# Kernel tuning notes

Hardware: AMD Instinct MI355X
Metric: run time of the kernel (lower is better)

## Reference

```python
import jax, jax.numpy as jnp
import numpy as np

H, DH = 8, 64          # heads, dim_head
SCALE = DH ** -0.5

def _ln(x, g, b, eps=1e-5):
    m = jnp.mean(x, axis=-1, keepdims=True)
    v = jnp.var(x, axis=-1, keepdims=True)
    return (x - m) / jnp.sqrt(v + eps) * g + b

def setup_inputs() -> dict:
    key = jax.random.key(0)
    ks = jax.random.split(key, 16)
    b, n, din, dim, depth, mlp, nc = 4, 2048, 768, 512, 2, 512, 2
    s = 0.02
    x = jax.random.normal(ks[0], (b, n, din), jnp.float32)
    lens = jax.random.randint(ks[1], (b,), n // 2, n + 1)
    lens = lens.at[0].set(n)  # ensure amax(lens) == n so torch's truncation is a no-op
    return {
        "x": x,
        "lens": lens,
        "cls_token": jax.random.normal(ks[2], (1, 1, dim), jnp.float32),
        "fc_w": jax.random.normal(ks[3], (din, dim), jnp.float32) * s,
        "fc_b": jnp.zeros((dim,), jnp.float32),
        "ln1_g": jnp.ones((depth, dim), jnp.float32),
        "ln1_b": jnp.zeros((depth, dim), jnp.float32),
        "qkv_w": jax.random.normal(ks[4], (depth, dim, 3 * H * DH), jnp.float32) * s,
        "out_w": jax.random.normal(ks[5], (depth, H * DH, dim), jnp.float32) * s,
        "out_b": jnp.zeros((depth, dim), jnp.float32),
        "ln2_g": jnp.ones((depth, dim), jnp.float32),
        "ln2_b": jnp.zeros((depth, dim), jnp.float32),
        "ff1_w": jax.random.normal(ks[6], (depth, dim, mlp), jnp.float32) * s,
        "ff1_b": jnp.zeros((depth, mlp), jnp.float32),
        "ff2_w": jax.random.normal(ks[7], (depth, mlp, dim), jnp.float32) * s,
        "ff2_b": jnp.zeros((depth, dim), jnp.float32),
        "lnf_g": jnp.ones((dim,), jnp.float32),
        "lnf_b": jnp.zeros((dim,), jnp.float32),
        "head_w": jax.random.normal(ks[8], (dim, nc), jnp.float32) * s,
        "head_b": jnp.zeros((nc,), jnp.float32),
    }

def reference(x, lens, cls_token, fc_w, fc_b, ln1_g, ln1_b, qkv_w, out_w, out_b,
              ln2_g, ln2_b, ff1_w, ff1_b, ff2_w, ff2_b, lnf_g, lnf_b, head_w, head_b):
    b, n, _ = x.shape
    # fc + GELU (exact erf gelu, matching torch nn.GELU default)
    x = jax.nn.gelu(x @ fc_w + fc_b, approximate=False)
    x = jnp.concatenate([jnp.broadcast_to(cls_token, (b, 1, x.shape[-1])), x], axis=1)
    n1 = n + 1
    lens1 = lens + 1
    # faithful mask: mask @ mask.mT -> True only where BOTH query and key are padding
    pad = jnp.arange(n1)[None, :] >= lens1[:, None]           # [b, n1]
    mask2 = pad[:, :, None] & pad[:, None, :]                  # [b, n1, n1]
    neg = -jnp.finfo(x.dtype).max
    depth = qkv_w.shape[0]
    for l in range(depth):
        xn = _ln(x, ln1_g[l], ln1_b[l])
        qkv = xn @ qkv_w[l]                                    # [b, n1, 3*H*DH]
        q, k, v = jnp.split(qkv, 3, axis=-1)
        q = q.reshape(b, n1, H, DH).transpose(0, 2, 1, 3)      # [b, h, n1, dh]
        k = k.reshape(b, n1, H, DH).transpose(0, 2, 1, 3)
        v = v.reshape(b, n1, H, DH).transpose(0, 2, 1, 3)
        dots = jnp.einsum('bhid,bhjd->bhij', q, k) * SCALE
        dots = jnp.where(mask2[:, None], neg, dots)
        dots = dots - jnp.max(dots, axis=-1, keepdims=True)
        attn = jax.nn.softmax(dots, axis=-1)
        o = jnp.einsum('bhij,bhjd->bhid', attn, v)
        o = o.transpose(0, 2, 1, 3).reshape(b, n1, H * DH)
        x = o @ out_w[l] + out_b[l] + x
        h = jax.nn.gelu(_ln(x, ln2_g[l], ln2_b[l]) @ ff1_w[l] + ff1_b[l], approximate=False)
        x = h @ ff2_w[l] + ff2_b[l] + x
    x = _ln(x, lnf_g, lnf_b)
    return x[:, 0] @ head_w + head_b   # pool='cls'
```

## Files before the change

kernel.cpp:

```cpp
#include <hip/hip_runtime.h>
#include <hip/hip_bf16.h>
#include <math.h>
#include <float.h>

typedef __hip_bfloat16 bf16;
using bf16x8 = __attribute__((ext_vector_type(8))) __bf16;
using f32x4  = __attribute__((ext_vector_type(4))) float;

constexpr int BATCH = 4;
constexpr int SEQ   = 2048;
constexpr int SEQ1  = 2049;
constexpr int DIN   = 768;
constexpr int DIMC  = 512;
constexpr int DEPTH = 2;
constexpr int NHEAD = 8;
constexpr int DHEAD = 64;
constexpr int ROWS  = BATCH * SEQ1;
constexpr int VKP   = 2112;
constexpr float ATT_SCALE = 0.125f;
constexpr float NEGBIG = -1e30f;

__device__ __forceinline__ bf16x8 ld_frag(const bf16* p) { return *(const bf16x8*)p; }

__device__ __forceinline__ void g2lds16(const bf16* g, bf16* l) {
    __builtin_amdgcn_global_load_lds(
        (const __attribute__((address_space(1))) void*)g,
        (__attribute__((address_space(3))) void*)l, 16, 0, 0);
}

__global__ __launch_bounds__(256) void cast_kernel(const float* __restrict__ src,
                                                   bf16* __restrict__ dst, int n4) {
    int i = blockIdx.x * 256 + threadIdx.x;
    if (i < n4) {
        float4 v = ((const float4*)src)[i];
        dst[i * 4 + 0] = __float2bfloat16(v.x);
        dst[i * 4 + 1] = __float2bfloat16(v.y);
        dst[i * 4 + 2] = __float2bfloat16(v.z);
        dst[i * 4 + 3] = __float2bfloat16(v.w);
    }
}

__global__ __launch_bounds__(256) void wt_transpose_kernel(
    const float* __restrict__ src, bf16* __restrict__ dst,
    int R, int C, long zstride) {
    __shared__ bf16 tile[32][33];
    int z = blockIdx.z;
    const float* s = src + (size_t)z * zstride;
    bf16* d = dst + (size_t)z * zstride;
    int tx = threadIdx.x, ty = threadIdx.y;
    int c0 = blockIdx.x * 32, r0 = blockIdx.y * 32;
    int c = c0 + tx;
#pragma unroll
    for (int rr = ty; rr < 32; rr += 8) {
        int r = r0 + rr;
        tile[rr][tx] = (r < R && c < C) ? __float2bfloat16(s[(size_t)r * C + c])
                                        : __float2bfloat16(0.f);
    }
    __syncthreads();
    int rc = r0 + tx;
#pragma unroll
    for (int cc = ty; cc < 32; cc += 8) {
        int oc = c0 + cc;
        if (rc < R && oc < C) d[(size_t)oc * R + rc] = tile[tx][cc];
    }
}

__global__ __launch_bounds__(256) void vt_transpose_kernel(
    const bf16* __restrict__ QKV, bf16* __restrict__ VT) {
    __shared__ bf16 tile[32][33];
    int z = blockIdx.z;
    int bb = z >> 3, hh = z & 7;
    const bf16* s = QKV + (size_t)bb * SEQ1 * 1536 + 1024 + hh * 64;
    bf16* d = VT + (size_t)z * 64 * VKP;
    int tx = threadIdx.x, ty = threadIdx.y;
    int c0 = blockIdx.x * 32, r0 = blockIdx.y * 32;
    int c = c0 + tx;
#pragma unroll
    for (int rr = ty; rr < 32; rr += 8) {
        int r = r0 + rr;
        tile[rr][tx] = (r < SEQ1) ? s[(size_t)r * 1536 + c] : __float2bfloat16(0.f);
    }
    __syncthreads();
    int rc = r0 + tx;
#pragma unroll
    for (int cc = ty; cc < 32; cc += 8) {
        int oc = c0 + cc;
        if (rc < VKP) d[(size_t)oc * VKP + rc] = tile[tx][cc];
    }
}

__global__ void cls_fill_kernel(const float* __restrict__ cls, float* __restrict__ X) {
    int b = blockIdx.x;
    for (int d = threadIdx.x; d < DIMC; d += blockDim.x)
        X[(size_t)b * SEQ1 * DIMC + d] = cls[d];
}

template<int BM, bool GELU_, bool RESID, bool REMAP, bool OBF>
__global__ __launch_bounds__(256) void gemm_bt(
    const bf16* __restrict__ A, const bf16* __restrict__ Bt,
    const float* __restrict__ bias, const float* __restrict__ resid,
    float* __restrict__ Cf, bf16* __restrict__ Ch, int M, int N, int K) {
    constexpr int MI = BM / 32;
    __shared__ __align__(16) bf16 As[BM * 32];
    __shared__ __align__(16) bf16 Bs[4096];
    int tid = threadIdx.x;
    int ln = tid & 63, wv = tid >> 6;
    int wr = wv >> 1, wc = wv & 1;
    int l15 = ln & 15, l4 = ln >> 4;
    int m0 = blockIdx.y * BM, n0 = blockIdx.x * 128;

    f32x4 acc[MI][4];
#pragma unroll
    for (int i = 0; i < MI; ++i)
#pragma unroll
        for (int j = 0; j < 4; ++j) acc[i][j] = {0.f, 0.f, 0.f, 0.f};

    int aslot[MI], bslot[4];
#pragma unroll
    for (int i = 0; i < MI; ++i) {
        int m = wr * (BM / 2) + i * 16 + l15;
        aslot[i] = m * 4 + (l4 ^ ((m >> 1) & 3));
    }
#pragma unroll
    for (int j = 0; j < 4; ++j) {
        int n = wc * 64 + j * 16 + l15;
        bslot[j] = n * 4 + (l4 ^ ((n >> 1) & 3));
    }

    for (int k0 = 0; k0 < K; k0 += 32) {
#pragma unroll
        for (int r = 0; r < BM / 64; ++r) {
            int s = r * 256 + tid;
            int m = s >> 2, c = s & 3;
            int kb = c ^ ((m >> 1) & 3);
            int gm = m0 + m; if (gm > M - 1) gm = M - 1;
            g2lds16(A + (size_t)gm * K + k0 + kb * 8, &As[s * 8]);
        }
#pragma unroll
        for (int r = 0; r < 2; ++r) {
            int s = r * 256 + tid;
            int n = s >> 2, c = s & 3;
            int kb = c ^ ((n >> 1) & 3);
            g2lds16(Bt + (size_t)(n0 + n) * K + k0 + kb * 8, &Bs[s * 8]);
        }
        __syncthreads();
        bf16x8 af[MI], bfr[4];
#pragma unroll
        for (int i = 0; i < MI; ++i) af[i] = ld_frag(&As[aslot[i] * 8]);
#pragma unroll
        for (int j = 0; j < 4; ++j) bfr[j] = ld_frag(&Bs[bslot[j] * 8]);
#pragma unroll
        for (int i = 0; i < MI; ++i)
#pragma unroll
            for (int j = 0; j < 4; ++j)
                acc[i][j] = __builtin_amdgcn_mfma_f32_16x16x32_bf16(af[i], bfr[j], acc[i][j], 0, 0, 0);
        __syncthreads();
    }

#pragma unroll
    for (int i = 0; i < MI; ++i) {
#pragma unroll
        for (int j = 0; j < 4; ++j) {
            int gn = n0 + wc * 64 + j * 16 + l15;
            float bb = bias ? bias[gn] : 0.f;
#pragma unroll
            for (int r = 0; r < 4; ++r) {
                int gm = m0 + wr * (BM / 2) + i * 16 + l4 * 4 + r;
                if (gm >= M) continue;
                float v = acc[i][j][r] + bb;
                if (GELU_) v = 0.5f * v * (1.f + erff(v * 0.70710678118654752f));
                size_t orow = gm;
                if (REMAP) { int b_ = gm >> 11; orow = (size_t)b_ * SEQ1 + (gm & 2047) + 1; }
                size_t oi = orow * (size_t)N + gn;
                if (RESID) v += resid[oi];
                if (OBF) Ch[oi] = __float2bfloat16(v); else Cf[oi] = v;
            }
        }
    }
}

__global__ __launch_bounds__(256) void ln_kernel(const float* __restrict__ Xin, bf16* __restrict__ Xout,
                          const float* __restrict__ g, const float* __restrict__ bb) {
    int wv = threadIdx.x >> 6, ln = threadIdx.x & 63;
    int row = blockIdx.x * 4 + wv;
    if (row >= ROWS) return;
    const float* xr = Xin + (size_t)row * DIMC + ln * 8;
    float4 a = *(const float4*)xr;
    float4 c = *(const float4*)(xr + 4);
    float s = a.x + a.y + a.z + a.w + c.x + c.y + c.z + c.w;
#pragma unroll
    for (int off = 1; off < 64; off <<= 1) s += __shfl_xor(s, off, 64);
    float mean = s * (1.f / 512.f);
    float d[8] = {a.x - mean, a.y - mean, a.z - mean, a.w - mean,
                  c.x - mean, c.y - mean, c.z - mean, c.w - mean};
    float var = 0.f;
#pragma unroll
    for (int e = 0; e < 8; ++e) var += d[e] * d[e];
#pragma unroll
    for (int off = 1; off < 64; off <<= 1) var += __shfl_xor(var, off, 64);
    float rinv = rsqrtf(var * (1.f / 512.f) + 1e-5f);
    const float* gp = g + ln * 8;
    const float* bp = bb + ln * 8;
    float4 g0 = *(const float4*)gp, g1 = *(const float4*)(gp + 4);
    float4 b0 = *(const float4*)bp, b1 = *(const float4*)(bp + 4);
    float gg[8] = {g0.x, g0.y, g0.z, g0.w, g1.x, g1.y, g1.z, g1.w};
    float bbv[8] = {b0.x, b0.y, b0.z, b0.w, b1.x, b1.y, b1.z, b1.w};
    union { unsigned short u[8]; uint4 v; } ou;
#pragma unroll
    for (int e = 0; e < 8; ++e)
        ou.u[e] = __builtin_bit_cast(unsigned short, __float2bfloat16(d[e] * rinv * gg[e] + bbv[e]));
    *(uint4*)(Xout + (size_t)row * DIMC + ln * 8) = ou.v;
}

__global__ __launch_bounds__(256, 5) void attn_kernel(
    const bf16* __restrict__ QKV, const bf16* __restrict__ VT,
    const int* __restrict__ lens, bf16* __restrict__ O) {
    __shared__ __align__(16) bf16 Ks[2][4096];
    __shared__ __align__(16) bf16 Vs[2][4096];
    int tid = threadIdx.x, ln = tid & 63, wv = tid >> 6;
    int l15 = ln & 15, l4 = ln >> 4;
    int q0 = blockIdx.x * 64, h = blockIdx.y, b = blockIdx.z;
    int len1 = lens[b] + 1;
    const bf16* qkv_b = QKV + (size_t)b * SEQ1 * 1536;
    const bf16* vt_b  = VT + (size_t)(b * 8 + h) * 64 * VKP;

    uint4 z4 = make_uint4(0u, 0u, 0u, 0u);
    uint4 q0v = z4, q1v = z4;
    int qrow = q0 + wv * 16 + l15;
    if (qrow < SEQ1) {
        const bf16* qp = qkv_b + (size_t)qrow * 1536 + h * 64 + l4 * 8;
        q0v = *(const uint4*)qp;
        q1v = *(const uint4*)(qp + 32);
    }
    bf16x8 bq0 = __builtin_bit_cast(bf16x8, q0v);
    bf16x8 bq1 = __builtin_bit_cast(bf16x8, q1v);
    bool qpad = (qrow >= len1);

    float mrun = NEGBIG, lrun = 0.f;
    f32x4 oaccT[4];
#pragma unroll
    for (int t = 0; t < 4; ++t) oaccT[t] = {0.f, 0.f, 0.f, 0.f};

    uint4 kr[2], vr[2];
    int srow[2], sseg[2];
    int kslot[2], vslot[2];
#pragma unroll
    for (int rr = 0; rr < 2; ++rr) {
        int idx = rr * 256 + tid;
        int row = idx >> 3, seg = idx & 7;
        srow[rr] = row; sseg[rr] = seg;
        int pb = row >> 5, w = row & 31;
        int krow = pb * 32 + ((w >> 2) & 1) * 16 + (w >> 3) * 4 + (w & 3);
        kslot[rr] = krow * 8 + (seg ^ (krow & 7));
        vslot[rr] = row * 8 + (seg ^ (row & 7));
    }

#pragma unroll
    for (int rr = 0; rr < 2; ++rr) {
        kr[rr] = (srow[rr] < SEQ1)
            ? *(const uint4*)(qkv_b + (size_t)srow[rr] * 1536 + 512 + h * 64 + sseg[rr] * 8) : z4;
        vr[rr] = *(const uint4*)(vt_b + (size_t)srow[rr] * VKP + sseg[rr] * 8);
    }
#pragma unroll
    for (int rr = 0; rr < 2; ++rr) {
        *(uint4*)&Ks[0][kslot[rr] * 8] = kr[rr];
        *(uint4*)&Vs[0][vslot[rr] * 8] = vr[rr];
    }
    __syncthreads();

    for (int kt = 0; kt < 33; ++kt) {
        int k0 = kt * 64;
        int buf = kt & 1;
        if (kt < 32) {
            int kn = k0 + 64;
#pragma unroll
            for (int rr = 0; rr < 2; ++rr) {
                kr[rr] = (kn + srow[rr] < SEQ1)
                    ? *(const uint4*)(qkv_b + (size_t)(kn + srow[rr]) * 1536 + 512 + h * 64 + sseg[rr] * 8) : z4;
                vr[rr] = *(const uint4*)(vt_b + (size_t)srow[rr] * VKP + kn + sseg[rr] * 8);
            }
        }

        f32x4 sacc[2][2];
#pragma unroll
        for (int pb = 0; pb < 2; ++pb)
#pragma unroll
            for (int s = 0; s < 2; ++s) {
                int R = pb * 32 + s * 16 + l15;
                f32x4 a = {0.f, 0.f, 0.f, 0.f};
                bf16x8 kf0 = ld_frag(&Ks[buf][(R * 8 + (l4 ^ (R & 7))) * 8]);
                bf16x8 kf1 = ld_frag(&Ks[buf][(R * 8 + ((l4 + 4) ^ (R & 7))) * 8]);
                a = __builtin_amdgcn_mfma_f32_16x16x32_bf16(kf0, bq0, a, 0, 0, 0);
                a = __builtin_amdgcn_mfma_f32_16x16x32_bf16(kf1, bq1, a, 0, 0, 0);
                sacc[pb][s] = a;
            }

        bool needmask = (k0 + 64 > len1) || (kt == 32);
        float sv[2][2][4];
        float mx = NEGBIG;
#pragma unroll
        for (int pb = 0; pb < 2; ++pb)
#pragma unroll
            for (int s = 0; s < 2; ++s)
#pragma unroll
                for (int r = 0; r < 4; ++r) {
                    float v = sacc[pb][s][r] * ATT_SCALE;
                    if (needmask) {
                        int j = k0 + pb * 32 + l4 * 8 + s * 4 + r;
                        if (j >= SEQ1 || (qpad && j >= len1)) v = NEGBIG;
                    }
                    sv[pb][s][r] = v;
                    mx = fmaxf(mx, v);
                }
        mx = fmaxf(mx, __shfl_xor(mx, 16, 64));
        mx = fmaxf(mx, __shfl_xor(mx, 32, 64));
        float mnew = fmaxf(mrun, mx);
        float alpha = __expf(mrun - mnew);
        float rs = 0.f;
        unsigned short pk[2][8];
#pragma unroll
        for (int pb = 0; pb < 2; ++pb)
#pragma unroll
            for (int s = 0; s < 2; ++s)
#pragma unroll
                for (int r = 0; r < 4; ++r) {
                    float ex = sv[pb][s][r] - mnew;
                    float p = (ex < -80.f) ? 0.f : __expf(ex);
                    rs += p;
                    pk[pb][s * 4 + r] = __builtin_bit_cast(unsigned short, __float2bfloat16(p));
                }
        rs += __shfl_xor(rs, 16, 64);
        rs += __shfl_xor(rs, 32, 64);
        lrun = lrun * alpha + rs;
        mrun = mnew;
#pragma unroll
        for (int t = 0; t < 4; ++t) {
            oaccT[t][0] *= alpha; oaccT[t][1] *= alpha;
            oaccT[t][2] *= alpha; oaccT[t][3] *= alpha;
        }

#pragma unroll
        for (int pb = 0; pb < 2; ++pb) {
            union { unsigned short u[8]; bf16x8 v; } pu;
#pragma unroll
            for (int e = 0; e < 8; ++e) pu.u[e] = pk[pb][e];
            bf16x8 pf = pu.v;
#pragma unroll
            for (int t = 0; t < 4; ++t) {
                int VR = t * 16 + l15;
                bf16x8 vf = ld_frag(&Vs[buf][(VR * 8 + ((pb * 4 + l4) ^ (VR & 7))) * 8]);
                oaccT[t] = __builtin_amdgcn_mfma_f32_16x16x32_bf16(vf, pf, oaccT[t], 0, 0, 0);
            }
        }

        if (kt < 32) {
            int ob = buf ^ 1;
#pragma unroll
            for (int rr = 0; rr < 2; ++rr) {
                *(uint4*)&Ks[ob][kslot[rr] * 8] = kr[rr];
                *(uint4*)&Vs[ob][vslot[rr] * 8] = vr[rr];
            }
        }
        __syncthreads();
    }

    if (qrow < SEQ1) {
        float rl = (lrun > 0.f) ? 1.f / lrun : 0.f;
        bf16* orow = O + ((size_t)b * SEQ1 + qrow) * DIMC + h * 64;
#pragma unroll
        for (int t = 0; t < 4; ++t) {
            union { unsigned short u[4]; uint2 v; } ou;
#pragma unroll
            for (int r = 0; r < 4; ++r)
                ou.u[r] = __builtin_bit_cast(unsigned short, __float2bfloat16(oaccT[t][r] * rl));
            *(uint2*)&orow[t * 16 + l4 * 4] = ou.v;
        }
    }
}

__global__ __launch_bounds__(256) void head_kernel(const float* __restrict__ X,
                            const float* __restrict__ g, const float* __restrict__ bb,
                            const float* __restrict__ hw, const float* __restrict__ hb,
                            float* __restrict__ out) {
    int b = blockIdx.x, t = threadIdx.x;
    const float* xr = X + (size_t)b * SEQ1 * DIMC;
    float v0 = xr[t], v1 = xr[t + 256];
    __shared__ float red[256];
    red[t] = v0 + v1;
    __syncthreads();
    for (int w = 128; w > 0; w >>= 1) { if (t < w) red[t] += red[t + w]; __syncthreads(); }
    float mean = red[0] * (1.f / 512.f);
    __syncthreads();
    float d0 = v0 - mean, d1 = v1 - mean;
    red[t] = d0 * d0 + d1 * d1;
    __syncthreads();
    for (int w = 128; w > 0; w >>= 1) { if (t < w) red[t] += red[t + w]; __syncthreads(); }
    float rinv = rsqrtf(red[0] * (1.f / 512.f) + 1e-5f);
    __syncthreads();
    float xn0 = d0 * rinv * g[t] + bb[t];
    float xn1 = d1 * rinv * g[t + 256] + bb[t + 256];
    float p0 = xn0 * hw[t * 2]     + xn1 * hw[(t + 256) * 2];
    float p1 = xn0 * hw[t * 2 + 1] + xn1 * hw[(t + 256) * 2 + 1];
    __shared__ float r0[256], r1[256];
    r0[t] = p0; r1[t] = p1;
    __syncthreads();
    for (int w = 128; w > 0; w >>= 1) { if (t < w) { r0[t] += r0[t + w]; r1[t] += r1[t + w]; } __syncthreads(); }
    if (t == 0) {
        out[b * 2 + 0] = r0[0] + hb[0];
        out[b * 2 + 1] = r1[0] + hb[1];
    }
}

extern "C" void kernel_launch(void* const* d_in, const int* in_sizes, int n_in,
                              void* d_out, int out_size, void* d_ws, size_t ws_size,
                              hipStream_t stream) {
    const float* x      = (const float*)d_in[0];
    const int*   lens   = (const int*)d_in[1];
    const float* cls    = (const float*)d_in[2];
    const float* fc_w   = (const float*)d_in[3];
    const float* fc_b   = (const float*)d_in[4];
    const float* ln1_g  = (const float*)d_in[5];
    const float* ln1_b  = (const float*)d_in[6];
    const float* qkv_w  = (const float*)d_in[7];
    const float* out_w  = (const float*)d_in[8];
    const float* out_b  = (const float*)d_in[9];
    const float* ln2_g  = (const float*)d_in[10];
    const float* ln2_b  = (const float*)d_in[11];
    const float* ff1_w  = (const float*)d_in[12];
    const float* ff1_b  = (const float*)d_in[13];
    const float* ff2_w  = (const float*)d_in[14];
    const float* ff2_b  = (const float*)d_in[15];
    const float* lnf_g  = (const float*)d_in[16];
    const float* lnf_b  = (const float*)d_in[17];
    const float* head_w = (const float*)d_in[18];
    const float* head_b = (const float*)d_in[19];
    float* out = (float*)d_out;

    char* w = (char*)d_ws;
    float* X    = (float*)w;  w += (size_t)ROWS * DIMC * 4;
    bf16*  XNh  = (bf16*)w;   w += (size_t)ROWS * DIMC * 2;
    bf16*  QKVh = (bf16*)w;   w += (size_t)ROWS * 1536 * 2;
    bf16*  Obh  = (bf16*)w;   w += (size_t)ROWS * DIMC * 2;
    bf16*  xbf  = (bf16*)w;   w += (size_t)BATCH * SEQ * DIN * 2;
    bf16*  VT   = xbf;
    bf16*  fc_wt  = (bf16*)w;
    bf16*  qkv_wt = fc_wt  + (size_t)DIN * DIMC;
    bf16*  out_wt = qkv_wt + (size_t)2 * DIMC * 1536;
    bf16*  ff1_wt = out_wt + (size_t)2 * DIMC * DIMC;
    bf16*  ff2_wt = ff1_wt + (size_t)2 * DIMC * DIMC;
    bf16*  Hbh  = Obh;

    dim3 blk(256);
    dim3 tb(32, 8);

    cast_kernel<<<dim3((BATCH * SEQ * DIN / 4 + 255) / 256), blk, 0, stream>>>(
        x, xbf, BATCH * SEQ * DIN / 4);

    wt_transpose_kernel<<<dim3(16, 24, 1), tb, 0, stream>>>(fc_w,  fc_wt,  DIN,  DIMC, (long)DIN * DIMC);
    wt_transpose_kernel<<<dim3(48, 16, 2), tb, 0, stream>>>(qkv_w, qkv_wt, DIMC, 1536, (long)DIMC * 1536);
    wt_transpose_kernel<<<dim3(16, 16, 2), tb, 0, stream>>>(out_w, out_wt, DIMC, DIMC, (long)DIMC * DIMC);
    wt_transpose_kernel<<<dim3(16, 16, 2), tb, 0, stream>>>(ff1_w, ff1_wt, DIMC, DIMC, (long)DIMC * DIMC);
    wt_transpose_kernel<<<dim3(16, 16, 2), tb, 0, stream>>>(ff2_w, ff2_wt, DIMC, DIMC, (long)DIMC * DIMC);

    gemm_bt<64, true, false, true, false><<<dim3(4, 128), blk, 0, stream>>>(
        xbf, fc_wt, fc_b, nullptr, X, nullptr, BATCH * SEQ, DIMC, DIN);
    cls_fill_kernel<<<dim3(BATCH), blk, 0, stream>>>(cls, X);

    for (int l = 0; l < DEPTH; ++l) {
        ln_kernel<<<dim3((ROWS + 3) / 4), blk, 0, stream>>>(X, XNh, ln1_g + l * DIMC, ln1_b + l * DIMC);
        gemm_bt<128, false, false, false, true><<<dim3(12, 65), blk, 0, stream>>>(
            XNh, qkv_wt + (size_t)l * DIMC * 1536, nullptr, nullptr, nullptr, QKVh, ROWS, 1536, DIMC);
        vt_transpose_kernel<<<dim3(2, 66, 32), tb, 0, stream>>>(QKVh, VT);
        attn_kernel<<<dim3(33, NHEAD, BATCH), blk, 0, stream>>>(QKVh, VT, lens, Obh);
        gemm_bt<64, false, true, false, false><<<dim3(4, 129), blk, 0, stream>>>(
            Obh, out_wt + (size_t)l * DIMC * DIMC, out_b + l * DIMC, X, X, nullptr, ROWS, DIMC, DIMC);
        ln_kernel<<<dim3((ROWS + 3) / 4), blk, 0, stream>>>(X, XNh, ln2_g + l * DIMC, ln2_b + l * DIMC);
        gemm_bt<64, true, false, false, true><<<dim3(4, 129), blk, 0, stream>>>(
            XNh, ff1_wt + (size_t)l * DIMC * DIMC, ff1_b + l * DIMC, nullptr, nullptr, Hbh, ROWS, DIMC, DIMC);
        gemm_bt<64, false, true, false, false><<<dim3(4, 129), blk, 0, stream>>>(
            Hbh, ff2_wt + (size_t)l * DIMC * DIMC, ff2_b + l * DIMC, X, X, nullptr, ROWS, DIMC, DIMC);
    }
    head_kernel<<<dim3(BATCH), blk, 0, stream>>>(X, lnf_g, lnf_b, head_w, head_b, out);
}
```

Before: 588.8 us.

## Flatten attention grid, precompute LDS offsets, and merge weight transposes

The attention grid becomes 1D with head and batch varying fastest, so blocks running at the same time share query-tile positions, which may improve L2 reuse of K/V. LDS fragment offsets and global K/V pointers are precomputed outside the loop, the separate score array is dropped in favour of reusing the accumulator registers, and the exp underflow guard is removed. The three square-weight transposes are merged into one launch. The changes lower address arithmetic, register pressure and launch count, with the small risk of behaviour changes from dropping the guard and the first-tile bounds check.

```diff
diff --git a/kernel.cpp b/kernel.cpp
--- a/kernel.cpp
+++ b/kernel.cpp
@@ -63,6 +63,27 @@
         int oc = c0 + cc;
         if (rc < R && oc < C) d[(size_t)oc * R + rc] = tile[tx][cc];
     }
+}
+
+__global__ __launch_bounds__(256) void wt3_transpose_kernel(
+    const float* __restrict__ w0, const float* __restrict__ w1, const float* __restrict__ w2,
+    bf16* __restrict__ dst) {
+    __shared__ bf16 tile[32][33];
+    int z = blockIdx.z;
+    const float* srcs[3] = {w0, w1, w2};
+    const float* s = srcs[z >> 1] + (size_t)(z & 1) * DIMC * DIMC;
+    bf16* d = dst + (size_t)z * DIMC * DIMC;
+    int tx = threadIdx.x, ty = threadIdx.y;
+    int c0 = blockIdx.x * 32, r0 = blockIdx.y * 32;
+    int c = c0 + tx;
+#pragma unroll
+    for (int rr = ty; rr < 32; rr += 8)
+        tile[rr][tx] = __float2bfloat16(s[(size_t)(r0 + rr) * DIMC + c]);
+    __syncthreads();
+    int rc = r0 + tx;
+#pragma unroll
+    for (int cc = ty; cc < 32; cc += 8)
+        d[(size_t)(c0 + cc) * DIMC + rc] = tile[tx][cc];
 }
 
 __global__ __launch_bounds__(256) void vt_transpose_kernel(
@@ -219,7 +240,8 @@
     __shared__ __align__(16) bf16 Vs[2][4096];
     int tid = threadIdx.x, ln = tid & 63, wv = tid >> 6;
     int l15 = ln & 15, l4 = ln >> 4;
-    int q0 = blockIdx.x * 64, h = blockIdx.y, b = blockIdx.z;
+    int bid = blockIdx.x;
+    int h = bid & 7, b = (bid >> 3) & 3, q0 = (bid >> 5) * 64;
     int len1 = lens[b] + 1;
     const bf16* qkv_b = QKV + (size_t)b * SEQ1 * 1536;
     const bf16* vt_b  = VT + (size_t)(b * 8 + h) * 64 * VKP;
@@ -241,43 +263,66 @@
 #pragma unroll
     for (int t = 0; t < 4; ++t) oaccT[t] = {0.f, 0.f, 0.f, 0.f};
 
+    int koff[2][2][2];
+#pragma unroll
+    for (int pb = 0; pb < 2; ++pb)
+#pragma unroll
+        for (int s = 0; s < 2; ++s) {
+            int R = pb * 32 + s * 16 + l15;
+            koff[pb][s][0] = (R * 8 + (l4 ^ (R & 7))) * 8;
+            koff[pb][s][1] = (R * 8 + ((l4 + 4) ^ (R & 7))) * 8;
+        }
+    int voff[2][4];
+#pragma unroll
+    for (int pb = 0; pb < 2; ++pb)
+#pragma unroll
+        for (int t = 0; t < 4; ++t) {
+            int VR = t * 16 + l15;
+            voff[pb][t] = (VR * 8 + ((pb * 4 + l4) ^ (VR & 7))) * 8;
+        }
+
     uint4 kr[2], vr[2];
-    int srow[2], sseg[2];
-    int kslot[2], vslot[2];
+    int srow[2], kslot[2], vslot[2];
+    const bf16* kg[2];
+    const bf16* vg[2];
 #pragma unroll
     for (int rr = 0; rr < 2; ++rr) {
         int idx = rr * 256 + tid;
         int row = idx >> 3, seg = idx & 7;
-        srow[rr] = row; sseg[rr] = seg;
+        srow[rr] = row;
         int pb = row >> 5, w = row & 31;
         int krow = pb * 32 + ((w >> 2) & 1) * 16 + (w >> 3) * 4 + (w & 3);
-        kslot[rr] = krow * 8 + (seg ^ (krow & 7));
-        vslot[rr] = row * 8 + (seg ^ (row & 7));
+        kslot[rr] = (krow * 8 + (seg ^ (krow & 7))) * 8;
+        vslot[rr] = (row * 8 + (seg ^ (row & 7))) * 8;
+        kg[rr] = qkv_b + (size_t)row * 1536 + 512 + h * 64 + seg * 8;
+        vg[rr] = vt_b + (size_t)row * VKP + seg * 8;
     }
 
 #pragma unroll
     for (int rr = 0; rr < 2; ++rr) {
-        kr[rr] = (srow[rr] < SEQ1)
-            ? *(const uint4*)(qkv_b + (size_t)srow[rr] * 1536 + 512 + h * 64 + sseg[rr] * 8) : z4;
-        vr[rr] = *(const uint4*)(vt_b + (size_t)srow[rr] * VKP + sseg[rr] * 8);
+        kr[rr] = *(const uint4*)kg[rr];
+        vr[rr] = *(const uint4*)vg[rr];
+        kg[rr] += 64 * 1536; vg[rr] += 64;
     }
 #pragma unroll
     for (int rr = 0; rr < 2; ++rr) {
-        *(uint4*)&Ks[0][kslot[rr] * 8] = kr[rr];
-        *(uint4*)&Vs[0][vslot[rr] * 8] = vr[rr];
+        *(uint4*)&Ks[0][kslot[rr]] = kr[rr];
+        *(uint4*)&Vs[0][vslot[rr]] = vr[rr];
     }
     __syncthreads();
 
     for (int kt = 0; kt < 33; ++kt) {
         int k0 = kt * 64;
         int buf = kt & 1;
+        const bf16* ksb = &Ks[buf][0];
+        const bf16* vsb = &Vs[buf][0];
         if (kt < 32) {
             int kn = k0 + 64;
 #pragma unroll
             for (int rr = 0; rr < 2; ++rr) {
-                kr[rr] = (kn + srow[rr] < SEQ1)
-                    ? *(const uint4*)(qkv_b + (size_t)(kn + srow[rr]) * 1536 + 512 + h * 64 + sseg[rr] * 8) : z4;
-                vr[rr] = *(const uint4*)(vt_b + (size_t)srow[rr] * VKP + kn + sseg[rr] * 8);
+                kr[rr] = (kn + srow[rr] < SEQ1) ? *(const uint4*)kg[rr] : z4;
+                vr[rr] = *(const uint4*)vg[rr];
+                kg[rr] += 64 * 1536; vg[rr] += 64;
             }
         }
 
@@ -286,17 +331,15 @@
         for (int pb = 0; pb < 2; ++pb)
 #pragma unroll
             for (int s = 0; s < 2; ++s) {
-                int R = pb * 32 + s * 16 + l15;
                 f32x4 a = {0.f, 0.f, 0.f, 0.f};
-                bf16x8 kf0 = ld_frag(&Ks[buf][(R * 8 + (l4 ^ (R & 7))) * 8]);
-                bf16x8 kf1 = ld_frag(&Ks[buf][(R * 8 + ((l4 + 4) ^ (R & 7))) * 8]);
+                bf16x8 kf0 = ld_frag(ksb + koff[pb][s][0]);
+                bf16x8 kf1 = ld_frag(ksb + koff[pb][s][1]);
                 a = __builtin_amdgcn_mfma_f32_16x16x32_bf16(kf0, bq0, a, 0, 0, 0);
                 a = __builtin_amdgcn_mfma_f32_16x16x32_bf16(kf1, bq1, a, 0, 0, 0);
                 sacc[pb][s] = a;
             }
 
         bool needmask = (k0 + 64 > len1) || (kt == 32);
-        float sv[2][2][4];
         float mx = NEGBIG;
 #pragma unroll
         for (int pb = 0; pb < 2; ++pb)
@@ -309,7 +352,7 @@
                         int j = k0 + pb * 32 + l4 * 8 + s * 4 + r;
                         if (j >= SEQ1 || (qpad && j >= len1)) v = NEGBIG;
                     }
-                    sv[pb][s][r] = v;
+                    sacc[pb][s][r] = v;
                     mx = fmaxf(mx, v);
                 }
         mx = fmaxf(mx, __shfl_xor(mx, 16, 64));
@@ -324,8 +367,7 @@
             for (int s = 0; s < 2; ++s)
 #pragma unroll
                 for (int r = 0; r < 4; ++r) {
-                    float ex = sv[pb][s][r] - mnew;
-                    float p = (ex < -80.f) ? 0.f : __expf(ex);
+                    float p = __expf(sacc[pb][s][r] - mnew);
                     rs += p;
                     pk[pb][s * 4 + r] = __builtin_bit_cast(unsigned short, __float2bfloat16(p));
                 }
@@ -347,18 +389,18 @@
             bf16x8 pf = pu.v;
 #pragma unroll
             for (int t = 0; t < 4; ++t) {
-                int VR = t * 16 + l15;
-                bf16x8 vf = ld_frag(&Vs[buf][(VR * 8 + ((pb * 4 + l4) ^ (VR & 7))) * 8]);
+                bf16x8 vf = ld_frag(vsb + voff[pb][t]);
                 oaccT[t] = __builtin_amdgcn_mfma_f32_16x16x32_bf16(vf, pf, oaccT[t], 0, 0, 0);
             }
         }
 
         if (kt < 32) {
-            int ob = buf ^ 1;
+            bf16* kob = &Ks[buf ^ 1][0];
+            bf16* vob = &Vs[buf ^ 1][0];
 #pragma unroll
             for (int rr = 0; rr < 2; ++rr) {
-                *(uint4*)&Ks[ob][kslot[rr] * 8] = kr[rr];
-                *(uint4*)&Vs[ob][vslot[rr] * 8] = vr[rr];
+                *(uint4*)&kob[kslot[rr]] = kr[rr];
+                *(uint4*)&vob[vslot[rr]] = vr[rr];
             }
         }
         __syncthreads();
@@ -458,9 +500,7 @@
 
     wt_transpose_kernel<<<dim3(16, 24, 1), tb, 0, stream>>>(fc_w,  fc_wt,  DIN,  DIMC, (long)DIN * DIMC);
     wt_transpose_kernel<<<dim3(48, 16, 2), tb, 0, stream>>>(qkv_w, qkv_wt, DIMC, 1536, (long)DIMC * 1536);
-    wt_transpose_kernel<<<dim3(16, 16, 2), tb, 0, stream>>>(out_w, out_wt, DIMC, DIMC, (long)DIMC * DIMC);
-    wt_transpose_kernel<<<dim3(16, 16, 2), tb, 0, stream>>>(ff1_w, ff1_wt, DIMC, DIMC, (long)DIMC * DIMC);
-    wt_transpose_kernel<<<dim3(16, 16, 2), tb, 0, stream>>>(ff2_w, ff2_wt, DIMC, DIMC, (long)DIMC * DIMC);
+    wt3_transpose_kernel<<<dim3(16, 16, 6), tb, 0, stream>>>(out_w, ff1_w, ff2_w, out_wt);
 
     gemm_bt<64, true, false, true, false><<<dim3(4, 128), blk, 0, stream>>>(
         xbf, fc_wt, fc_b, nullptr, X, nullptr, BATCH * SEQ, DIMC, DIN);
@@ -471,7 +511,7 @@
         gemm_bt<128, false, false, false, true><<<dim3(12, 65), blk, 0, stream>>>(
             XNh, qkv_wt + (size_t)l * DIMC * 1536, nullptr, nullptr, nullptr, QKVh, ROWS, 1536, DIMC);
         vt_transpose_kernel<<<dim3(2, 66, 32), tb, 0, stream>>>(QKVh, VT);
-        attn_kernel<<<dim3(33, NHEAD, BATCH), blk, 0, stream>>>(QKVh, VT, lens, Obh);
+        attn_kernel<<<dim3(1056), blk, 0, stream>>>(QKVh, VT, lens, Obh);
         gemm_bt<64, false, true, false, false><<<dim3(4, 129), blk, 0, stream>>>(
             Obh, out_wt + (size_t)l * DIMC * DIMC, out_b + l * DIMC, X, X, nullptr, ROWS, DIMC, DIMC);
         ln_kernel<<<dim3((ROWS + 3) / 4), blk, 0, stream>>>(X, XNh, ln2_g + l * DIMC, ln2_b + l * DIMC);
```

New measurement: 750.2 us. 1.27x slower.
